# Kernel optimization log

Measured on AMD Instinct MI355X. Metric: run time of the kernel, lower is better.

Reference implementation:

```python
import jax, jax.numpy as jnp
import numpy as np

LOG2 = float(np.log(2.0))

def _ssp(x):
    # shifted softplus: ln(0.5*(exp(x)+1)) = softplus(x) - ln 2
    return jax.nn.softplus(x) - LOG2

def setup_inputs() -> dict:
    key = jax.random.key(0)
    ks = jax.random.split(key, 8)
    B, N, D = 32, 512, 1024
    H = D // 2
    s = lambda fan_in: 1.0 / np.sqrt(fan_in)
    return {
        "representation": jax.random.normal(ks[0], (B, N, D), jnp.float32),
        "R": jax.random.normal(ks[1], (B, N, 3), jnp.float32),
        "atom_mask": jnp.ones((B, N), jnp.float32),
        "W1": jax.random.normal(ks[2], (D, H), jnp.float32) * s(D),
        "b1": jnp.zeros((H,), jnp.float32),
        "W2": jax.random.normal(ks[3], (H, 1), jnp.float32) * s(H),
        "b2": jnp.zeros((1,), jnp.float32),
        "Wc1": jax.random.normal(ks[4], (D, H), jnp.float32) * s(D),
        "bc1": jnp.zeros((H,), jnp.float32),
        "Wc2": jax.random.normal(ks[5], (H, 1), jnp.float32) * s(H),
        "bc2": jnp.zeros((1,), jnp.float32),
    }

def reference(representation, R, atom_mask, W1, b1, W2, b2, Wc1, bc1, Wc2, bc2):
    B, N, _ = representation.shape
    # Atomwise pyramidal MLP: n_in -> n_in//2 (shifted softplus) -> 1
    yi = _ssp(jnp.einsum("bnd,dh->bnh", representation, W1) + b1)
    yi = jnp.einsum("bnh,ho->bno", yi, W2) + b2            # [B,N,1]
    # masked sum pool over atoms (mean=0, stddev=1 so standardize is identity)
    y = jnp.sum(yi * atom_mask[..., None], axis=1)          # [B,1]

    # pairwise distances with safe sqrt (diag is exactly zero)
    diff = R[:, None, :, :] - R[:, :, None, :]              # [B,N,N,3]
    d2 = jnp.sum(diff * diff, axis=-1)                      # [B,N,N]
    dist = jnp.where(d2 > 0, jnp.sqrt(jnp.where(d2 > 0, d2, 1.0)), 0.0)

    eye = jnp.eye(N, dtype=dist.dtype)
    tot_mask = atom_mask[:, None, :] * atom_mask[:, :, None] * (1.0 - eye)
    keep = (tot_mask != 0).astype(dist.dtype)               # [B,N,N]
    dist = dist * keep

    # charge net: Dense(n_in, n_in//2, ssp) -> Dense(n_in//2, 1)
    q = _ssp(jnp.einsum("bnd,dh->bnh", representation, Wc1) + bc1)
    q = jnp.einsum("bnh,ho->bno", q, Wc2) + bc2             # [B,N,1]

    inv2 = (1e-5 + dist) ** -2                              # [B,N,N]
    coulomb = q[:, :, 0][:, None, :] * inv2 * q             # [B,N,N] (q_j * inv * q_i)
    coulomb = coulomb * keep
    e = jnp.sum(coulomb, axis=(1, 2))                       # [B]

    return y + e[:, None]                                   # [B,1]
```

## Files before the change

### kernel.cpp

```cpp
#include <hip/hip_runtime.h>
#include <math.h>


typedef unsigned short u16;
typedef unsigned int u32;
typedef __bf16 bf16x8 __attribute__((ext_vector_type(8)));
typedef float f32x4 __attribute__((ext_vector_type(4)));

#define GK 1024
#define NT 16

#define GLOAD_LDS16(g, l) __builtin_amdgcn_global_load_lds( \
    (const __attribute__((address_space(1))) void*)(g),     \
    (__attribute__((address_space(3))) void*)(l), 16, 0, 0)

__device__ __forceinline__ u16 f2bf(float f) {
    u32 u = __float_as_uint(f);
    return (u16)((u + 0x7FFFu + ((u >> 16) & 1u)) >> 16);
}

__device__ __forceinline__ float ssp_f(float x) {
    return __logf(0.5f * (__expf(x) + 1.0f));
}

__device__ __forceinline__ float ssp_slow(float x) {
    return fmaxf(x, 0.0f) + log1pf(expf(-fabsf(x))) - 0.6931471805599453f;
}


__global__ __launch_bounds__(256) void prep(
    const float* __restrict__ rep, const float* __restrict__ W1,
    const float* __restrict__ Wc1, u16* __restrict__ Abf,
    u16* __restrict__ Btb, float* __restrict__ out)
{
    __shared__ float tile[32][33];
    const int blk = blockIdx.x;
    const int t = threadIdx.x;
    if (blk < 8192) {
        int i = (blk * 256 + t) * 8;
        float4 x = *(const float4*)(rep + i);
        float4 y = *(const float4*)(rep + i + 4);
        union { u16 h[8]; uint4 v; } o;
        o.h[0] = f2bf(x.x); o.h[1] = f2bf(x.y); o.h[2] = f2bf(x.z); o.h[3] = f2bf(x.w);
        o.h[4] = f2bf(y.x); o.h[5] = f2bf(y.y); o.h[6] = f2bf(y.z); o.h[7] = f2bf(y.w);
        *(uint4*)(Abf + i) = o.v;
        if (blk == 0 && t < 32) out[t] = 0.0f;
    } else {
        const int bb = blk - 8192;
        const int k0 = (bb & 31) * 32;
        const int n0 = (bb >> 5) * 32;
        const float* src = (n0 < 512) ? W1 : Wc1;
        const int ns0 = (n0 < 512) ? n0 : n0 - 512;
#pragma unroll
        for (int j = 0; j < 4; j++) {
            int idx = j * 256 + t;
            int kl = idx >> 5, nl = idx & 31;
            tile[kl][nl] = src[(size_t)(k0 + kl) * 512 + ns0 + nl];
        }
        __syncthreads();
#pragma unroll
        for (int j = 0; j < 4; j++) {
            int idx = j * 256 + t;
            int nl = idx >> 5, kl = idx & 31;
            Btb[(size_t)(n0 + nl) * 1024 + k0 + kl] = f2bf(tile[kl][nl]);
        }
    }
}


__global__ __launch_bounds__(512, 2) void gemm_mfma(
    const u16* __restrict__ A,
    const u16* __restrict__ Bt,
    const float* __restrict__ b1, const float* __restrict__ W2,
    const float* __restrict__ bc1, const float* __restrict__ Wc2,
    float* __restrict__ parts)
{
    __shared__ u16 smem[2][32768];

    const int blk = blockIdx.x;
    const int swz = ((blk & 7) << 5) | (blk >> 3);
    const int bm = swz >> 2;
    const int bn = swz & 3;
    const int tid = threadIdx.x;
    const int w = tid >> 6, lane = tid & 63;
    const int wm = w & 1, wn = w >> 1;
    const int lm = lane & 15, q = lane >> 4;

    f32x4 acc[8][4];
#pragma unroll
    for (int i = 0; i < 8; i++)
#pragma unroll
        for (int j = 0; j < 4; j++)
            acc[i][j] = (f32x4){0.0f, 0.0f, 0.0f, 0.0f};

    int goffA[2][2], goffB[2][2];
#pragma unroll
    for (int h = 0; h < 2; h++)
#pragma unroll
        for (int p2 = 0; p2 < 2; p2++) {
            int ci = h * 1024 + (w * 2 + p2) * 64 + lane;
            int s = ci >> 3;
            int c = (ci & 7) ^ (s & 7);
            int gA = (s & 63) + ((s >> 6) & 1) * 128 + ((s >> 7) & 1) * 64;
            int gB = (s & 31) + ((s >> 5) & 3) * 64 + ((s >> 7) & 1) * 32;
            goffA[h][p2] = gA * GK + c * 8;
            goffB[h][p2] = gB * GK + c * 8;
        }

    const int aswz0 = (q ^ (lm & 7)) * 8;
    const int aswz1 = ((4 + q) ^ (lm & 7)) * 8;
    const u32 base0 = (u32)(size_t)(__attribute__((address_space(3))) void*)&smem[0][0];
    const u32 aA0 = base0 + 2u * (u32)((wm * 64 + lm) * 64 + aswz0);
    const u32 aA1 = base0 + 2u * (u32)((wm * 64 + lm) * 64 + aswz1);
    const u32 bB0 = base0 + 32768u + 2u * (u32)((wn * 32 + lm) * 64 + aswz0);
    const u32 bB1 = base0 + 32768u + 2u * (u32)((wn * 32 + lm) * 64 + aswz1);
    const u32 aA0b = aA0 + 65536u, aA1b = aA1 + 65536u;
    const u32 bB0b = bB0 + 65536u, bB1b = bB1 + 65536u;

    const u16* Ab = A + (size_t)bm * 256 * GK;
    const u16* Bb = Bt + (size_t)bn * 256 * GK;

#define STAGE2(G, RG, H, BUF, GOFF) do {                                      \
    GLOAD_LDS16((G) + GOFF[H][0], &smem[BUF][(RG) + ((H) * 1024 + (w * 2 + 0) * 64) * 8]); \
    GLOAD_LDS16((G) + GOFF[H][1], &smem[BUF][(RG) + ((H) * 1024 + (w * 2 + 1) * 64) * 8]); \
} while (0)

#define DSR(D, AD, O) asm volatile("ds_read_b128 %0, %1 offset:" #O          \
                                   : "=v"(D) : "v"(AD))

#define RD_A0(F, R0, R1) do {                                                 \
    DSR(F[0][0], R0, 0);     DSR(F[0][1], R1, 0);                             \
    DSR(F[1][0], R0, 2048);  DSR(F[1][1], R1, 2048);                          \
    DSR(F[2][0], R0, 4096);  DSR(F[2][1], R1, 4096);                          \
    DSR(F[3][0], R0, 6144);  DSR(F[3][1], R1, 6144); } while (0)

#define RD_A1(F, R0, R1) do {                                                 \
    DSR(F[0][0], R0, 16384); DSR(F[0][1], R1, 16384);                         \
    DSR(F[1][0], R0, 18432); DSR(F[1][1], R1, 18432);                         \
    DSR(F[2][0], R0, 20480); DSR(F[2][1], R1, 20480);                         \
    DSR(F[3][0], R0, 22528); DSR(F[3][1], R1, 22528); } while (0)

#define RD_B0(F, R0, R1) do {                                                 \
    DSR(F[0][0], R0, 0);     DSR(F[0][1], R1, 0);                             \
    DSR(F[1][0], R0, 2048);  DSR(F[1][1], R1, 2048); } while (0)

#define RD_B1(F, R0, R1) do {                                                 \
    DSR(F[0][0], R0, 16384); DSR(F[0][1], R1, 16384);                         \
    DSR(F[1][0], R0, 18432); DSR(F[1][1], R1, 18432); } while (0)

#define MFMA_Q(MH, NH, AF, BF)                                                \
    _Pragma("unroll") for (int kk = 0; kk < 2; kk++)                          \
    _Pragma("unroll") for (int mi = 0; mi < 4; mi++)                          \
    _Pragma("unroll") for (int nj = 0; nj < 2; nj++)                          \
        acc[(MH) * 4 + mi][(NH) * 2 + nj] = __builtin_amdgcn_mfma_f32_16x16x32_bf16( \
            AF[mi][kk], BF[nj][kk], acc[(MH) * 4 + mi][(NH) * 2 + nj], 0, 0, 0);

#define WAITV4 do { asm volatile("s_waitcnt vmcnt(4)" ::: "memory");          \
                    __builtin_amdgcn_sched_barrier(0); } while (0)
#define LGKM0  do { asm volatile("s_waitcnt lgkmcnt(0)" ::: "memory");        \
                    __builtin_amdgcn_sched_barrier(0); } while (0)

#define TILE(RA0, RA1, RB0, RB1, SB, GAN, GBN) do {                           \
                                                                 \
    STAGE2(GAN, 0, 0, SB, goffA);                                             \
    RD_A0(afr, RA0, RA1);                                                     \
    RD_B0(b0f, RB0, RB1);                                                     \
    __builtin_amdgcn_s_barrier();                                             \
    LGKM0;                                                                    \
    __builtin_amdgcn_s_setprio(1);                                            \
    MFMA_Q(0, 0, afr, b0f);                                                   \
    __builtin_amdgcn_s_setprio(0);                                            \
    WAITV4;                                                                   \
    __builtin_amdgcn_s_barrier();                                             \
                                                                 \
    STAGE2(GBN, 16384, 0, SB, goffB);                                         \
    RD_B1(b1f, RB0, RB1);                                                     \
    __builtin_amdgcn_s_barrier();                                             \
    LGKM0;                                                                    \
    __builtin_amdgcn_s_setprio(1);                                            \
    MFMA_Q(0, 1, afr, b1f);                                                   \
    __builtin_amdgcn_s_setprio(0);                                            \
    WAITV4;                                                                   \
    __builtin_amdgcn_s_barrier();                                             \
                                                           \
    STAGE2(GBN, 16384, 1, SB, goffB);                                         \
    STAGE2(GAN, 0, 1, SB, goffA);                                             \
    RD_A1(afr, RA0, RA1);                                                     \
    __builtin_amdgcn_s_barrier();                                             \
    LGKM0;                                                                    \
    __builtin_amdgcn_s_setprio(1);                                            \
    MFMA_Q(1, 1, afr, b1f);                                                   \
    MFMA_Q(1, 0, afr, b0f);                                                   \
    __builtin_amdgcn_s_setprio(0);                                            \
    WAITV4;                                                                   \
    __builtin_amdgcn_s_barrier();                                             \
} while (0)

    bf16x8 afr[4][2], b0f[2][2], b1f[2][2];

    STAGE2(Ab, 0, 0, 0, goffA);
    STAGE2(Bb, 16384, 0, 0, goffB);
    STAGE2(Bb, 16384, 1, 0, goffB);
    STAGE2(Ab, 0, 1, 0, goffA);
    WAITV4;
    __builtin_amdgcn_s_barrier();

    for (int tt = 0; tt < 8; ++tt) {
        const u16* gA0 = Ab + ((2 * tt + 1) & (NT - 1)) * 64;
        const u16* gB0 = Bb + ((2 * tt + 1) & (NT - 1)) * 64;
        const u16* gA1 = Ab + ((2 * tt + 2) & (NT - 1)) * 64;
        const u16* gB1 = Bb + ((2 * tt + 2) & (NT - 1)) * 64;
        TILE(aA0, aA1, bB0, bB1, 1, gA0, gB0);
        TILE(aA0b, aA1b, bB0b, bB1b, 0, gA1, gB1);
    }

    asm volatile("s_waitcnt vmcnt(0)" ::: "memory");

#undef STAGE2
#undef DSR
#undef RD_A0
#undef RD_A1
#undef RD_B0
#undef RD_B1
#undef MFMA_Q
#undef WAITV4
#undef LGKM0
#undef TILE

    __syncthreads();
    float* red = (float*)&smem[0][0];
    const bool is_q = (bn >= 2);
    const float* bb2 = is_q ? bc1 : b1;
    const float* vv = is_q ? Wc2 : W2;
    float bias[4], v[4];
#pragma unroll
    for (int nfr = 0; nfr < 4; nfr++) {
        int c = (bn & 1) * 256 + wn * 64 + nfr * 16 + lm;
        bias[nfr] = bb2[c];
        v[nfr] = vv[c];
    }
#pragma unroll
    for (int mfr = 0; mfr < 8; mfr++) {
#pragma unroll
        for (int r = 0; r < 4; r++) {
            float s = 0.0f;
#pragma unroll
            for (int nfr = 0; nfr < 4; nfr++)
                s += v[nfr] * ssp_f(acc[mfr][nfr][r] + bias[nfr]);
            s += __shfl_xor(s, 1);
            s += __shfl_xor(s, 2);
            s += __shfl_xor(s, 4);
            s += __shfl_xor(s, 8);
            if (lm == 0) red[wn * 256 + wm * 128 + mfr * 16 + q * 4 + r] = s;
        }
    }
    __syncthreads();
    if (tid < 256) {
        float val = red[0 * 256 + tid] + red[1 * 256 + tid] +
                    red[2 * 256 + tid] + red[3 * 256 + tid];
        parts[(size_t)bn * 16384 + bm * 256 + tid] = val;
    }
}


__global__ __launch_bounds__(256) void coulomb_k(
    const float* __restrict__ R, const float* __restrict__ mask,
    const float* __restrict__ parts, const float* __restrict__ b2p,
    const float* __restrict__ bc2p, float* __restrict__ out)
{
    const int N = 512;
    const int b = blockIdx.y;
    const int chunk = blockIdx.x;
    __shared__ float Rx[512], Ry[512], Rz[512], QM[512];
    __shared__ float rbuf[4];
    const int tid = threadIdx.x;
    const float bc2 = bc2p[0];
    const float b2 = b2p[0];

    for (int j = tid; j < N; j += 256) {
        int idx = b * N + j;
        float m = mask[idx];
        const float* rp = R + (size_t)idx * 3;
        Rx[j] = rp[0];
        Ry[j] = rp[1];
        Rz[j] = rp[2];
        float qv = parts[2 * 16384 + idx] + parts[3 * 16384 + idx] + bc2;
        QM[j] = qv * m;
    }
    __syncthreads();

    const int i = chunk * 64 + (tid & 63);
    const int js = (tid >> 6) * 128;
    const float xi = Rx[i], yi = Ry[i], zi = Rz[i], qmi = QM[i];
    float e = 0.0f;
    for (int j = js; j < js + 128; j++) {
        float dx = xi - Rx[j];
        float dy = yi - Ry[j];
        float dz = zi - Rz[j];
        float d2 = dx * dx + dy * dy + dz * dz;
        float t = 1e-5f + sqrtf(d2);
        float term = qmi * QM[j] / (t * t);
        e += (j == i) ? 0.0f : term;
    }
    if (tid < 64) {
        int ii = b * N + chunk * 64 + tid;
        float yv = parts[0 * 16384 + ii] + parts[1 * 16384 + ii] + b2;
        e += yv * mask[ii];
    }
    for (int off = 32; off > 0; off >>= 1) e += __shfl_down(e, off, 64);
    if ((tid & 63) == 0) rbuf[tid >> 6] = e;
    __syncthreads();
    if (tid == 0) atomicAdd(&out[b], rbuf[0] + rbuf[1] + rbuf[2] + rbuf[3]);
}


#define BM 128
#define BN 64
#define BK 16

__global__ __launch_bounds__(256) void mlp_gemm(
    const float* __restrict__ A, const float* __restrict__ W1,
    const float* __restrict__ Wc1, const float* __restrict__ b1,
    const float* __restrict__ bc1, const float* __restrict__ W2,
    const float* __restrict__ Wc2, float* __restrict__ yi_part,
    float* __restrict__ q_part)
{
    const int K = 1024;
    const int bm = blockIdx.x;
    const int bn = blockIdx.y;
    const bool is_q = (bn >= 8);
    const float* __restrict__ W = is_q ? Wc1 : W1;
    const int j0 = (bn & 7) * BN;

    __shared__ float As[BK][BM + 4];
    __shared__ float Bs[BK][BN + 4];
    __shared__ float red[BM];

    const int tid = threadIdx.x;
    const int tx = tid & 15;
    const int ty = tid >> 4;

    float acc[8][4];
#pragma unroll
    for (int r = 0; r < 8; r++)
#pragma unroll
        for (int c = 0; c < 4; c++) acc[r][c] = 0.0f;

    const int a_row = tid >> 2;
    const int a_k4 = (tid & 3) * 4;
    const float* Arow0 = A + (size_t)(bm * BM + a_row) * K;
    const float* Arow1 = Arow0 + (size_t)64 * K;
    const int w_k = tid >> 4;
    const int w_j = (tid & 15) * 4;

    for (int kt = 0; kt < K; kt += BK) {
        float4 av0 = *(const float4*)(Arow0 + kt + a_k4);
        float4 av1 = *(const float4*)(Arow1 + kt + a_k4);
        float4 wv = *(const float4*)(W + (size_t)(kt + w_k) * 512 + j0 + w_j);
        __syncthreads();
        As[a_k4 + 0][a_row] = av0.x;
        As[a_k4 + 1][a_row] = av0.y;
        As[a_k4 + 2][a_row] = av0.z;
        As[a_k4 + 3][a_row] = av0.w;
        As[a_k4 + 0][a_row + 64] = av1.x;
        As[a_k4 + 1][a_row + 64] = av1.y;
        As[a_k4 + 2][a_row + 64] = av1.z;
        As[a_k4 + 3][a_row + 64] = av1.w;
        *(float4*)&Bs[w_k][w_j] = wv;
        __syncthreads();
#pragma unroll
        for (int kk = 0; kk < BK; kk++) {
            float4 a0v = *(const float4*)&As[kk][ty * 8];
            float4 a1v = *(const float4*)&As[kk][ty * 8 + 4];
            float4 bv = *(const float4*)&Bs[kk][tx * 4];
            float ar[8] = {a0v.x, a0v.y, a0v.z, a0v.w, a1v.x, a1v.y, a1v.z, a1v.w};
            float bc[4] = {bv.x, bv.y, bv.z, bv.w};
#pragma unroll
            for (int r = 0; r < 8; r++)
#pragma unroll
                for (int c = 0; c < 4; c++)
                    acc[r][c] = fmaf(ar[r], bc[c], acc[r][c]);
        }
    }

    const float* bb = is_q ? bc1 : b1;
    const float* vv = is_q ? Wc2 : W2;
    float bias[4], v[4];
#pragma unroll
    for (int c = 0; c < 4; c++) {
        bias[c] = bb[j0 + tx * 4 + c];
        v[c] = vv[j0 + tx * 4 + c];
    }
    if (tid < BM) red[tid] = 0.0f;
    __syncthreads();
#pragma unroll
    for (int r = 0; r < 8; r++) {
        float s = 0.0f;
#pragma unroll
        for (int c = 0; c < 4; c++)
            s += v[c] * ssp_slow(acc[r][c] + bias[c]);
        atomicAdd(&red[ty * 8 + r], s);
    }
    __syncthreads();
    float* target = is_q ? q_part : yi_part;
    if (tid < BM) atomicAdd(&target[(size_t)bm * BM + tid], red[tid]);
}

__global__ __launch_bounds__(256) void coulomb_fb(
    const float* __restrict__ R, const float* __restrict__ mask,
    const float* __restrict__ yi_part, const float* __restrict__ q_part,
    const float* __restrict__ b2p, const float* __restrict__ bc2p,
    float* __restrict__ out)
{
    const int N = 512;
    const int b = blockIdx.y;
    const int chunk = blockIdx.x;
    __shared__ float Rx[512], Ry[512], Rz[512], QM[512];
    __shared__ float rbuf[4];
    const int tid = threadIdx.x;
    const float bc2 = bc2p[0];
    const float b2 = b2p[0];

    for (int j = tid; j < N; j += 256) {
        float m = mask[b * N + j];
        const float* rp = R + ((size_t)b * N + j) * 3;
        Rx[j] = rp[0];
        Ry[j] = rp[1];
        Rz[j] = rp[2];
        QM[j] = (q_part[b * N + j] + bc2) * m;
    }
    __syncthreads();

    const int i = chunk * 64 + (tid & 63);
    const int js = (tid >> 6) * 128;
    const float xi = Rx[i], yi = Ry[i], zi = Rz[i], qmi = QM[i];
    float e = 0.0f;
    for (int j = js; j < js + 128; j++) {
        float dx = xi - Rx[j];
        float dy = yi - Ry[j];
        float dz = zi - Rz[j];
        float d2 = dx * dx + dy * dy + dz * dz;
        float t = 1e-5f + sqrtf(d2);
        float term = qmi * QM[j] / (t * t);
        e += (j == i) ? 0.0f : term;
    }
    if (tid < 64) {
        int ii = chunk * 64 + tid;
        e += (yi_part[b * N + ii] + b2) * mask[b * N + ii];
    }
    for (int off = 32; off > 0; off >>= 1) e += __shfl_down(e, off, 64);
    if ((tid & 63) == 0) rbuf[tid >> 6] = e;
    __syncthreads();
    if (tid == 0) atomicAdd(&out[b], rbuf[0] + rbuf[1] + rbuf[2] + rbuf[3]);
}


extern "C" void kernel_launch(void* const* d_in, const int* in_sizes, int n_in,
                              void* d_out, int out_size, void* d_ws, size_t ws_size,
                              hipStream_t stream) {
    const float* rep  = (const float*)d_in[0];
    const float* R    = (const float*)d_in[1];
    const float* mask = (const float*)d_in[2];
    const float* W1   = (const float*)d_in[3];
    const float* b1   = (const float*)d_in[4];
    const float* W2   = (const float*)d_in[5];
    const float* b2   = (const float*)d_in[6];
    const float* Wc1  = (const float*)d_in[7];
    const float* bc1  = (const float*)d_in[8];
    const float* Wc2  = (const float*)d_in[9];
    const float* bc2  = (const float*)d_in[10];
    float* out = (float*)d_out;

    const size_t szA = 16384ull * 1024 * 2;
    const size_t szB = 1024ull * 1024 * 2;
    const size_t szP = 8ull * 16384 * 4;
    const size_t need = szA + szB + szP;

    if (ws_size >= need) {
        u16* Abf = (u16*)d_ws;
        u16* Btb = (u16*)((char*)d_ws + szA);
        float* parts = (float*)((char*)d_ws + szA + szB);

        prep<<<8192 + 1024, 256, 0, stream>>>(rep, W1, Wc1, Abf, Btb, out);
        gemm_mfma<<<256, 512, 0, stream>>>(Abf, Btb, b1, W2, bc1, Wc2, parts);
        coulomb_k<<<dim3(8, 32), 256, 0, stream>>>(R, mask, parts, b2, bc2, out);
    } else {
        float* yi_part = (float*)d_ws;
        float* q_part = yi_part + 16384;
        hipMemsetAsync(d_ws, 0, 2 * 16384 * sizeof(float), stream);
        hipMemsetAsync(d_out, 0, 32 * sizeof(float), stream);
        mlp_gemm<<<dim3(128, 16), 256, 0, stream>>>(rep, W1, Wc1, b1, bc1, W2, Wc2,
                                                    yi_part, q_part);
        coulomb_fb<<<dim3(8, 32), 256, 0, stream>>>(R, mask, yi_part, q_part, b2, bc2, out);
    }
}
```

Measured before the change: 168.5 us.

## Restructure GEMM LDS layout and deepen global-to-LDS prefetch pipeline

Changes the LDS tile layout from an interleaved row mapping to contiguous 128-row halves for A and B, which simplifies the global offsets to one per lane pair. Global-to-LDS loads are rescheduled so that half-tiles for the next and next-next K steps are issued across four phases of each tile. The issuing keeps more loads in flight (vmcnt 6 instead of 4) and adds an extra barrier phase. The goal is better overlap of memory latency with MFMA work. The cost is tighter synchronisation and a risk of LDS write-after-read hazards if the buffer reuse ordering is wrong.

After: 167.0 us. Within noise of the previous version (-0.9%).

```diff
diff --git a/kernel.cpp b/kernel.cpp
--- a/kernel.cpp
+++ b/kernel.cpp
@@ -93,137 +93,134 @@
         for (int j = 0; j < 4; j++)
             acc[i][j] = (f32x4){0.0f, 0.0f, 0.0f, 0.0f};
 
-    int goffA[2][2], goffB[2][2];
-#pragma unroll
-    for (int h = 0; h < 2; h++)
-#pragma unroll
-        for (int p2 = 0; p2 < 2; p2++) {
-            int ci = h * 1024 + (w * 2 + p2) * 64 + lane;
-            int s = ci >> 3;
-            int c = (ci & 7) ^ (s & 7);
-            int gA = (s & 63) + ((s >> 6) & 1) * 128 + ((s >> 7) & 1) * 64;
-            int gB = (s & 31) + ((s >> 5) & 3) * 64 + ((s >> 7) & 1) * 32;
-            goffA[h][p2] = gA * GK + c * 8;
-            goffB[h][p2] = gB * GK + c * 8;
-        }
-
-    const int aswz0 = (q ^ (lm & 7)) * 8;
-    const int aswz1 = ((4 + q) ^ (lm & 7)) * 8;
+    int soff[2];
+#pragma unroll
+    for (int p2 = 0; p2 < 2; p2++) {
+        int ci = (w * 2 + p2) * 64 + lane;
+        int s = ci >> 3;
+        int c = (ci & 7) ^ (s & 7);
+        soff[p2] = s * GK + c * 8;
+    }
+
+    const int swz0 = (q ^ (lm & 7)) * 16;
+    const int swz1 = ((4 + q) ^ (lm & 7)) * 16;
     const u32 base0 = (u32)(size_t)(__attribute__((address_space(3))) void*)&smem[0][0];
-    const u32 aA0 = base0 + 2u * (u32)((wm * 64 + lm) * 64 + aswz0);
-    const u32 aA1 = base0 + 2u * (u32)((wm * 64 + lm) * 64 + aswz1);
-    const u32 bB0 = base0 + 32768u + 2u * (u32)((wn * 32 + lm) * 64 + aswz0);
-    const u32 bB1 = base0 + 32768u + 2u * (u32)((wn * 32 + lm) * 64 + aswz1);
-    const u32 aA0b = aA0 + 65536u, aA1b = aA1 + 65536u;
-    const u32 bB0b = bB0 + 65536u, bB1b = bB1 + 65536u;
+    const u32 xA0 = base0 + (u32)(wm * 16384 + lm * 128 + swz0);
+    const u32 xA1 = base0 + (u32)(wm * 16384 + lm * 128 + swz1);
+    const u32 xB0 = base0 + (u32)(32768 + (wn >> 1) * 16384 + ((wn & 1) * 64 + lm) * 128 + swz0);
+    const u32 xB1 = base0 + (u32)(32768 + (wn >> 1) * 16384 + ((wn & 1) * 64 + lm) * 128 + swz1);
+    const u32 yA0 = xA0 + 65536u, yA1 = xA1 + 65536u;
+    const u32 yB0 = xB0 + 65536u, yB1 = xB1 + 65536u;
 
     const u16* Ab = A + (size_t)bm * 256 * GK;
     const u16* Bb = Bt + (size_t)bn * 256 * GK;
 
-#define STAGE2(G, RG, H, BUF, GOFF) do {                                      \
-    GLOAD_LDS16((G) + GOFF[H][0], &smem[BUF][(RG) + ((H) * 1024 + (w * 2 + 0) * 64) * 8]); \
-    GLOAD_LDS16((G) + GOFF[H][1], &smem[BUF][(RG) + ((H) * 1024 + (w * 2 + 1) * 64) * 8]); \
+#define STAGE_H(G, T, H, BUF, REGU16) do {                                    \
+    const u16* g_ = (G) + (size_t)(H) * 128 * GK + (size_t)(T) * 64;          \
+    GLOAD_LDS16(g_ + soff[0], &smem[BUF][(REGU16) + (w * 2 + 0) * 512]);      \
+    GLOAD_LDS16(g_ + soff[1], &smem[BUF][(REGU16) + (w * 2 + 1) * 512]);      \
 } while (0)
 
 #define DSR(D, AD, O) asm volatile("ds_read_b128 %0, %1 offset:" #O          \
                                    : "=v"(D) : "v"(AD))
 
-#define RD_A0(F, R0, R1) do {                                                 \
-    DSR(F[0][0], R0, 0);     DSR(F[0][1], R1, 0);                             \
-    DSR(F[1][0], R0, 2048);  DSR(F[1][1], R1, 2048);                          \
-    DSR(F[2][0], R0, 4096);  DSR(F[2][1], R1, 4096);                          \
-    DSR(F[3][0], R0, 6144);  DSR(F[3][1], R1, 6144); } while (0)
-
-#define RD_A1(F, R0, R1) do {                                                 \
-    DSR(F[0][0], R0, 16384); DSR(F[0][1], R1, 16384);                         \
-    DSR(F[1][0], R0, 18432); DSR(F[1][1], R1, 18432);                         \
-    DSR(F[2][0], R0, 20480); DSR(F[2][1], R1, 20480);                         \
-    DSR(F[3][0], R0, 22528); DSR(F[3][1], R1, 22528); } while (0)
-
-#define RD_B0(F, R0, R1) do {                                                 \
-    DSR(F[0][0], R0, 0);     DSR(F[0][1], R1, 0);                             \
-    DSR(F[1][0], R0, 2048);  DSR(F[1][1], R1, 2048); } while (0)
-
-#define RD_B1(F, R0, R1) do {                                                 \
-    DSR(F[0][0], R0, 16384); DSR(F[0][1], R1, 16384);                         \
-    DSR(F[1][0], R0, 18432); DSR(F[1][1], R1, 18432); } while (0)
-
-#define MFMA_Q(MH, NH, AF, BF)                                                \
+#define RD_AQ0(F, A0k, A1k) do {                                              \
+    DSR(F[0][0], A0k, 0);     DSR(F[0][1], A1k, 0);                           \
+    DSR(F[1][0], A0k, 2048);  DSR(F[1][1], A1k, 2048);                        \
+    DSR(F[2][0], A0k, 4096);  DSR(F[2][1], A1k, 4096);                        \
+    DSR(F[3][0], A0k, 6144);  DSR(F[3][1], A1k, 6144); } while (0)
+
+#define RD_AQ1(F, A0k, A1k) do {                                              \
+    DSR(F[0][0], A0k, 8192);  DSR(F[0][1], A1k, 8192);                        \
+    DSR(F[1][0], A0k, 10240); DSR(F[1][1], A1k, 10240);                       \
+    DSR(F[2][0], A0k, 12288); DSR(F[2][1], A1k, 12288);                       \
+    DSR(F[3][0], A0k, 14336); DSR(F[3][1], A1k, 14336); } while (0)
+
+#define RD_BQ0(F, B0k, B1k) do {                                              \
+    DSR(F[0][0], B0k, 0);     DSR(F[0][1], B1k, 0);                           \
+    DSR(F[1][0], B0k, 2048);  DSR(F[1][1], B1k, 2048); } while (0)
+
+#define RD_BQ1(F, B0k, B1k) do {                                              \
+    DSR(F[0][0], B0k, 4096);  DSR(F[0][1], B1k, 4096);                        \
+    DSR(F[1][0], B0k, 6144);  DSR(F[1][1], B1k, 6144); } while (0)
+
+#define MFMA_Q(QM, QN, AF, BF)                                                \
     _Pragma("unroll") for (int kk = 0; kk < 2; kk++)                          \
     _Pragma("unroll") for (int mi = 0; mi < 4; mi++)                          \
     _Pragma("unroll") for (int nj = 0; nj < 2; nj++)                          \
-        acc[(MH) * 4 + mi][(NH) * 2 + nj] = __builtin_amdgcn_mfma_f32_16x16x32_bf16( \
-            AF[mi][kk], BF[nj][kk], acc[(MH) * 4 + mi][(NH) * 2 + nj], 0, 0, 0);
-
-#define WAITV4 do { asm volatile("s_waitcnt vmcnt(4)" ::: "memory");          \
-                    __builtin_amdgcn_sched_barrier(0); } while (0)
-#define LGKM0  do { asm volatile("s_waitcnt lgkmcnt(0)" ::: "memory");        \
-                    __builtin_amdgcn_sched_barrier(0); } while (0)
-
-#define TILE(RA0, RA1, RB0, RB1, SB, GAN, GBN) do {                           \
-                                                                 \
-    STAGE2(GAN, 0, 0, SB, goffA);                                             \
-    RD_A0(afr, RA0, RA1);                                                     \
-    RD_B0(b0f, RB0, RB1);                                                     \
+        acc[(QM) * 4 + mi][(QN) * 2 + nj] = __builtin_amdgcn_mfma_f32_16x16x32_bf16( \
+            AF[mi][kk], BF[nj][kk], acc[(QM) * 4 + mi][(QN) * 2 + nj], 0, 0, 0);
+
+#define LGKM0 do { asm volatile("s_waitcnt lgkmcnt(0)" ::: "memory");         \
+                   __builtin_amdgcn_sched_barrier(0); } while (0)
+
+#define TILE(CUR, NXT, A0k, A1k, B0k, B1k, T) do {                            \
+                               \
+    STAGE_H(Ab, ((T) + 1) & (NT - 1), 1, NXT, 8192);                          \
+    RD_AQ0(afr, A0k, A1k);                                                    \
+    RD_BQ0(b0f, B0k, B1k);                                                    \
     __builtin_amdgcn_s_barrier();                                             \
     LGKM0;                                                                    \
     __builtin_amdgcn_s_setprio(1);                                            \
     MFMA_Q(0, 0, afr, b0f);                                                   \
     __builtin_amdgcn_s_setprio(0);                                            \
-    WAITV4;                                                                   \
-    __builtin_amdgcn_s_barrier();                                             \
-                                                                 \
-    STAGE2(GBN, 16384, 0, SB, goffB);                                         \
-    RD_B1(b1f, RB0, RB1);                                                     \
+    __builtin_amdgcn_s_barrier();                                             \
+                                                           \
+    RD_BQ1(b1f, B0k, B1k);                                                    \
     __builtin_amdgcn_s_barrier();                                             \
     LGKM0;                                                                    \
     __builtin_amdgcn_s_setprio(1);                                            \
     MFMA_Q(0, 1, afr, b1f);                                                   \
     __builtin_amdgcn_s_setprio(0);                                            \
-    WAITV4;                                                                   \
-    __builtin_amdgcn_s_barrier();                                             \
-                                                           \
-    STAGE2(GBN, 16384, 1, SB, goffB);                                         \
-    STAGE2(GAN, 0, 1, SB, goffA);                                             \
-    RD_A1(afr, RA0, RA1);                                                     \
+    __builtin_amdgcn_s_barrier();                                             \
+             \
+    STAGE_H(Bb, ((T) + 2) & (NT - 1), 0, CUR, 16384);                         \
+    RD_AQ1(afr, A0k, A1k);                                                    \
     __builtin_amdgcn_s_barrier();                                             \
     LGKM0;                                                                    \
     __builtin_amdgcn_s_setprio(1);                                            \
     MFMA_Q(1, 1, afr, b1f);                                                   \
+    __builtin_amdgcn_s_setprio(0);                                            \
+    __builtin_amdgcn_s_barrier();                                             \
+    \
+    STAGE_H(Bb, ((T) + 2) & (NT - 1), 1, CUR, 24576);                         \
+    STAGE_H(Ab, ((T) + 2) & (NT - 1), 0, CUR, 0);                             \
+    __builtin_amdgcn_s_setprio(1);                                            \
     MFMA_Q(1, 0, afr, b0f);                                                   \
     __builtin_amdgcn_s_setprio(0);                                            \
-    WAITV4;                                                                   \
+    asm volatile("s_waitcnt vmcnt(6)" ::: "memory");                          \
+    __builtin_amdgcn_sched_barrier(0);                                        \
     __builtin_amdgcn_s_barrier();                                             \
 } while (0)
 
     bf16x8 afr[4][2], b0f[2][2], b1f[2][2];
 
-    STAGE2(Ab, 0, 0, 0, goffA);
-    STAGE2(Bb, 16384, 0, 0, goffB);
-    STAGE2(Bb, 16384, 1, 0, goffB);
-    STAGE2(Ab, 0, 1, 0, goffA);
-    WAITV4;
+    STAGE_H(Ab, 0, 0, 0, 0);
+    STAGE_H(Ab, 0, 1, 0, 8192);
+    STAGE_H(Bb, 0, 0, 0, 16384);
+    STAGE_H(Bb, 0, 1, 0, 24576);
+    STAGE_H(Bb, 1, 0, 1, 16384);
+    STAGE_H(Bb, 1, 1, 1, 24576);
+    STAGE_H(Ab, 1, 0, 1, 0);
+    asm volatile("s_waitcnt vmcnt(6)" ::: "memory");
+    __builtin_amdgcn_sched_barrier(0);
     __builtin_amdgcn_s_barrier();
 
     for (int tt = 0; tt < 8; ++tt) {
-        const u16* gA0 = Ab + ((2 * tt + 1) & (NT - 1)) * 64;
-        const u16* gB0 = Bb + ((2 * tt + 1) & (NT - 1)) * 64;
-        const u16* gA1 = Ab + ((2 * tt + 2) & (NT - 1)) * 64;
-        const u16* gB1 = Bb + ((2 * tt + 2) & (NT - 1)) * 64;
-        TILE(aA0, aA1, bB0, bB1, 1, gA0, gB0);
-        TILE(aA0b, aA1b, bB0b, bB1b, 0, gA1, gB1);
+        const int t0 = 2 * tt, t1 = 2 * tt + 1;
+        TILE(0, 1, xA0, xA1, xB0, xB1, t0);
+        TILE(1, 0, yA0, yA1, yB0, yB1, t1);
     }
 
     asm volatile("s_waitcnt vmcnt(0)" ::: "memory");
 
-#undef STAGE2
+#undef STAGE_H
 #undef DSR
-#undef RD_A0
-#undef RD_A1
-#undef RD_B0
-#undef RD_B1
+#undef RD_AQ0
+#undef RD_AQ1
+#undef RD_BQ0
+#undef RD_BQ1
 #undef MFMA_Q
-#undef WAITV4
 #undef LGKM0
 #undef TILE
 
```
